# Kernel optimization log

Hardware: AMD Instinct MI355X
Metric: run time of the kernel (lower is better)

## Reference

```python
import jax, jax.numpy as jnp
import numpy as np

B, S, IN, N, OUT = 16, 4096, 256, 256, 256
EPS = 1e-5

def setup_inputs() -> dict:
    key = jax.random.key(0)
    ks = jax.random.split(key, 6)
    return {
        "u": jax.random.normal(ks[0], (B, S, IN), dtype=jnp.float32),
        "A": jax.random.normal(ks[1], (N, N), dtype=jnp.float32) * 0.05,
        "B_w": jax.random.normal(ks[2], (N, IN), dtype=jnp.float32) * (1.0 / np.sqrt(IN)),
        "B_b": jax.random.normal(ks[3], (N,), dtype=jnp.float32) * 0.01,
        "ln_g": jnp.ones((N,), dtype=jnp.float32),
        "ln_b": jnp.zeros((N,), dtype=jnp.float32),
        "C_w": jax.random.normal(ks[4], (OUT, N), dtype=jnp.float32) * (1.0 / np.sqrt(N)),
        "C_b": jax.random.normal(ks[5], (OUT,), dtype=jnp.float32) * 0.01,
    }

def _layernorm(x, g, b):
    mu = jnp.mean(x, axis=-1, keepdims=True)
    var = jnp.mean(jnp.square(x - mu), axis=-1, keepdims=True)
    return (x - mu) * jax.lax.rsqrt(var + EPS) * g + b

def reference(u, A, B_w, B_b, ln_g, ln_b, C_w, C_b):
    # Precompute input injection B(u_t) for all t: [B, S, N]
    Bu = jnp.einsum('bsi,ni->bsn', u, B_w) + B_b
    state0 = jnp.zeros((u.shape[0], A.shape[0]), dtype=u.dtype)

    def step(state, bu_t):
        s = state @ A.T + bu_t          # [B, N]
        s = _layernorm(s, ln_g, ln_b)
        s = jax.nn.relu(s)
        return s, s

    _, states_t = jax.lax.scan(step, state0, jnp.swapaxes(Bu, 0, 1))  # [S, B, N]
    states = jnp.swapaxes(states_t, 0, 1)                              # [B, S, N]
    outputs = jnp.einsum('bsn,on->bso', states, C_w) + C_b             # [B, S, OUT]
    return states, outputs
```

## Files before the change

kernel.cpp:

```cpp
#include <hip/hip_runtime.h>

#define B_DIM 16
#define S_DIM 4096
#define N_DIM 256
#define EPS 1e-5f

__global__ __launch_bounds__(256)
void gemm_xwT_bias(const float* __restrict__ X,
                   const float* __restrict__ W,
                   const float* __restrict__ bias,
                   float* __restrict__ Y,
                   int M)
{
    __shared__ float Xs[16][68];
    __shared__ float Ws[16][68];

    const int tid = threadIdx.x;
    const int m0 = blockIdx.x * 64;
    const int n0 = blockIdx.y * 64;
    const int tx = tid & 15;
    const int ty = tid >> 4;

    float acc[4][4] = {};

    for (int k0 = 0; k0 < 256; k0 += 16) {
        {
            const int r  = tid >> 2;
            const int kk = (tid & 3) * 4;
            float4 v = *(const float4*)(X + (size_t)(m0 + r) * 256 + k0 + kk);
            Xs[kk + 0][r] = v.x; Xs[kk + 1][r] = v.y;
            Xs[kk + 2][r] = v.z; Xs[kk + 3][r] = v.w;
            float4 w = *(const float4*)(W + (size_t)(n0 + r) * 256 + k0 + kk);
            Ws[kk + 0][r] = w.x; Ws[kk + 1][r] = w.y;
            Ws[kk + 2][r] = w.z; Ws[kk + 3][r] = w.w;
        }
        __syncthreads();

        #pragma unroll
        for (int k = 0; k < 16; ++k) {
            float4 xv = *(const float4*)&Xs[k][ty * 4];
            float4 wv = *(const float4*)&Ws[k][tx * 4];
            float xa[4] = {xv.x, xv.y, xv.z, xv.w};
            float wa[4] = {wv.x, wv.y, wv.z, wv.w};
            #pragma unroll
            for (int i = 0; i < 4; ++i)
                #pragma unroll
                for (int j = 0; j < 4; ++j)
                    acc[i][j] += xa[i] * wa[j];
        }
        __syncthreads();
    }

    const int nbase = n0 + tx * 4;
    float4 bv = *(const float4*)(bias + nbase);
    #pragma unroll
    for (int i = 0; i < 4; ++i) {
        const int m = m0 + ty * 4 + i;
        float4 o;
        o.x = acc[i][0] + bv.x;
        o.y = acc[i][1] + bv.y;
        o.z = acc[i][2] + bv.z;
        o.w = acc[i][3] + bv.w;
        *(float4*)(Y + (size_t)m * 256 + nbase) = o;
    }
}

template<int CTRL>
__device__ __forceinline__ float dpp_term(float x) {
    return __int_as_float(
        __builtin_amdgcn_update_dpp(0, __float_as_int(x), CTRL, 0xF, 0xF, true));
}

__device__ __forceinline__ float wave_sum_l63(float v) {
    v += dpp_term<0x111>(v);
    v += dpp_term<0x112>(v);
    v += dpp_term<0x114>(v);
    v += dpp_term<0x118>(v);
    v += dpp_term<0x142>(v);
    v += dpp_term<0x143>(v);
    return v;
}

__device__ __forceinline__ float readlane63(float x) {
    return __int_as_float(__builtin_amdgcn_readlane(__float_as_int(x), 63));
}

__global__ __launch_bounds__(512, 2)
void scan_kernel(const float* __restrict__ A,
                 const float* __restrict__ Bu,
                 const float* __restrict__ ln_g,
                 const float* __restrict__ ln_b,
                 float* __restrict__ states)
{
    const int b = blockIdx.x;
    const int t = threadIdx.x;
    const int w = t >> 6;
    const int l = t & 63;

    __shared__ float s_state[256];
    __shared__ float s_partial[8][256];

    float4 a4[4][8];
    #pragma unroll
    for (int j = 0; j < 4; ++j) {
        const float* arow = A + (size_t)(4 * l + j) * 256 + 32 * w;
        #pragma unroll
        for (int c = 0; c < 8; ++c)
            a4[j][c] = ((const float4*)arow)[c];
    }

    const bool red = (w == 0);

    const float* bu_base  = Bu + (size_t)b * S_DIM * N_DIM;
    float*       out_base = states + (size_t)b * S_DIM * N_DIM;

    float4 g4  = make_float4(0.f, 0.f, 0.f, 0.f);
    float4 be4 = g4;
    float4 bu0 = g4, bu1 = g4;
    if (red) {
        g4  = ((const float4*)ln_g)[l];
        be4 = ((const float4*)ln_b)[l];
        bu0 = ((const float4*)bu_base)[l];
        bu1 = ((const float4*)(bu_base + N_DIM))[l];
        ((float4*)s_state)[l] = make_float4(0.f, 0.f, 0.f, 0.f);
    }
    __syncthreads();

    for (int step = 0; step < S_DIM; ++step) {
        float4 bu2 = make_float4(0.f, 0.f, 0.f, 0.f);
        if (red && (step + 2 < S_DIM))
            bu2 = ((const float4*)(bu_base + (size_t)(step + 2) * N_DIM))[l];

        const float4* sp = (const float4*)(s_state + 32 * w);
        float accA[4] = {0.f, 0.f, 0.f, 0.f};
        float accB[4] = {0.f, 0.f, 0.f, 0.f};
        #pragma unroll
        for (int c = 0; c < 8; ++c) {
            const float4 sc = sp[c];
            #pragma unroll
            for (int j = 0; j < 4; ++j) {
                const float4 a = a4[j][c];
                if (c & 1) {
                    accB[j] = fmaf(a.x, sc.x, accB[j]);
                    accB[j] = fmaf(a.y, sc.y, accB[j]);
                    accB[j] = fmaf(a.z, sc.z, accB[j]);
                    accB[j] = fmaf(a.w, sc.w, accB[j]);
                } else {
                    accA[j] = fmaf(a.x, sc.x, accA[j]);
                    accA[j] = fmaf(a.y, sc.y, accA[j]);
                    accA[j] = fmaf(a.z, sc.z, accA[j]);
                    accA[j] = fmaf(a.w, sc.w, accA[j]);
                }
            }
        }
        float4 pr;
        pr.x = accA[0] + accB[0];
        pr.y = accA[1] + accB[1];
        pr.z = accA[2] + accB[2];
        pr.w = accA[3] + accB[3];
        *(float4*)&s_partial[w][4 * l] = pr;

        asm volatile("s_waitcnt lgkmcnt(0)" ::: "memory");
        __builtin_amdgcn_s_barrier();

        if (red) {
            const float* prow = &s_partial[0][4 * l];
            const float4 q0 = *(const float4*)(prow + 0 * 256);
            const float4 q1 = *(const float4*)(prow + 1 * 256);
            const float4 q2 = *(const float4*)(prow + 2 * 256);
            const float4 q3 = *(const float4*)(prow + 3 * 256);
            const float4 q4 = *(const float4*)(prow + 4 * 256);
            const float4 q5 = *(const float4*)(prow + 5 * 256);
            const float4 q6 = *(const float4*)(prow + 6 * 256);
            const float4 q7 = *(const float4*)(prow + 7 * 256);

            float4 v;
            v.x = ((q0.x + q1.x) + (q2.x + q3.x)) + ((q4.x + q5.x) + (q6.x + q7.x)) + bu0.x;
            v.y = ((q0.y + q1.y) + (q2.y + q3.y)) + ((q4.y + q5.y) + (q6.y + q7.y)) + bu0.y;
            v.z = ((q0.z + q1.z) + (q2.z + q3.z)) + ((q4.z + q5.z) + (q6.z + q7.z)) + bu0.z;
            v.w = ((q0.w + q1.w) + (q2.w + q3.w)) + ((q4.w + q5.w) + (q6.w + q7.w)) + bu0.w;

            const float sv = (v.x + v.y) + (v.z + v.w);
            const float sq = fmaf(v.x, v.x, fmaf(v.y, v.y, fmaf(v.z, v.z, v.w * v.w)));

            const float tot  = readlane63(wave_sum_l63(sv));
            const float tot2 = readlane63(wave_sum_l63(sq));

            const float mu  = tot * (1.0f / 256.0f);
            const float var = tot2 * (1.0f / 256.0f) - mu * mu;
            const float inv = rsqrtf(var + EPS);

            float4 y;
            y.x = fmaxf((v.x - mu) * inv * g4.x + be4.x, 0.0f);
            y.y = fmaxf((v.y - mu) * inv * g4.y + be4.y, 0.0f);
            y.z = fmaxf((v.z - mu) * inv * g4.z + be4.z, 0.0f);
            y.w = fmaxf((v.w - mu) * inv * g4.w + be4.w, 0.0f);

            ((float4*)s_state)[l] = y;
            *(float4*)(out_base + (size_t)step * N_DIM + 4 * l) = y;

            bu0 = bu1;
            bu1 = bu2;
        }

        asm volatile("s_waitcnt lgkmcnt(0)" ::: "memory");
        __builtin_amdgcn_s_barrier();
    }
}

extern "C" void kernel_launch(void* const* d_in, const int* in_sizes, int n_in,
                              void* d_out, int out_size, void* d_ws, size_t ws_size,
                              hipStream_t stream)
{
    const float* u    = (const float*)d_in[0];
    const float* A    = (const float*)d_in[1];
    const float* B_w  = (const float*)d_in[2];
    const float* B_b  = (const float*)d_in[3];
    const float* ln_g = (const float*)d_in[4];
    const float* ln_b = (const float*)d_in[5];
    const float* C_w  = (const float*)d_in[6];
    const float* C_b  = (const float*)d_in[7];

    float* states  = (float*)d_out;
    float* outputs = (float*)d_out + (size_t)B_DIM * S_DIM * N_DIM;

    float* Bu = outputs;

    const int M = B_DIM * S_DIM;

    {
        dim3 grid(M / 64, N_DIM / 64);
        hipLaunchKernelGGL(gemm_xwT_bias, grid, dim3(256), 0, stream,
                           u, B_w, B_b, Bu, M);
    }

    {
        hipLaunchKernelGGL(scan_kernel, dim3(B_DIM), dim3(512), 0, stream,
                           A, Bu, ln_g, ln_b, states);
    }

    {
        dim3 grid(M / 64, N_DIM / 64);
        hipLaunchKernelGGL(gemm_xwT_bias, grid, dim3(256), 0, stream,
                           states, C_w, C_b, outputs, M);
    }
}
```

Before: 3.150 ms.

## Repartition scan matvec across 1024 threads with distributed LayerNorm reduction

Each scan block now runs 1024 threads. Each output row is split across 4 lane groups that reduce with cross-lane shuffles, replacing the layout where 8 waves wrote partial sums to shared memory and a single wave reduced them. LayerNorm statistics are computed per wave with DPP row sums and combined through a small shared array, so every thread normalizes its own element. This removes the serial single-wave reduction phase that ran between barriers. In exchange it uses more threads per block and makes more redundant reads of the statistics array.

```diff
diff --git a/kernel.cpp b/kernel.cpp
--- a/kernel.cpp
+++ b/kernel.cpp
@@ -71,21 +71,15 @@
         __builtin_amdgcn_update_dpp(0, __float_as_int(x), CTRL, 0xF, 0xF, true));
 }
 
-__device__ __forceinline__ float wave_sum_l63(float v) {
+__device__ __forceinline__ float row_sum_l15(float v) {
     v += dpp_term<0x111>(v);
     v += dpp_term<0x112>(v);
     v += dpp_term<0x114>(v);
     v += dpp_term<0x118>(v);
-    v += dpp_term<0x142>(v);
-    v += dpp_term<0x143>(v);
     return v;
 }
 
-__device__ __forceinline__ float readlane63(float x) {
-    return __int_as_float(__builtin_amdgcn_readlane(__float_as_int(x), 63));
-}
-
-__global__ __launch_bounds__(512, 2)
+__global__ __launch_bounds__(1024, 4)
 void scan_kernel(const float* __restrict__ A,
                  const float* __restrict__ Bu,
                  const float* __restrict__ ln_g,
@@ -96,115 +90,99 @@
     const int t = threadIdx.x;
     const int w = t >> 6;
     const int l = t & 63;
-
-    __shared__ float s_state[256];
-    __shared__ float s_partial[8][256];
-
-    float4 a4[4][8];
+    const int r = l >> 4;
+    const int c = l & 15;
+    const int o = 16 * w + c;
+
+    __shared__ __align__(16) float  s4[4 * 68];
+    __shared__ __align__(16) float2 s_red[16];
+
+    float4 a4[16];
+    {
+        const float* arow = A + (size_t)o * 256 + 64 * r;
+        #pragma unroll
+        for (int i = 0; i < 16; ++i)
+            a4[i] = ((const float4*)arow)[i];
+    }
     #pragma unroll
-    for (int j = 0; j < 4; ++j) {
-        const float* arow = A + (size_t)(4 * l + j) * 256 + 32 * w;
-        #pragma unroll
-        for (int c = 0; c < 8; ++c)
-            a4[j][c] = ((const float4*)arow)[c];
-    }
-
-    const bool red = (w == 0);
+    for (int i = 0; i < 16; ++i)
+        asm volatile("" : "+v"(a4[i].x), "+v"(a4[i].y),
+                          "+v"(a4[i].z), "+v"(a4[i].w));
+
+    const float g    = ln_g[o];
+    const float beta = ln_b[o];
 
     const float* bu_base  = Bu + (size_t)b * S_DIM * N_DIM;
     float*       out_base = states + (size_t)b * S_DIM * N_DIM;
 
-    float4 g4  = make_float4(0.f, 0.f, 0.f, 0.f);
-    float4 be4 = g4;
-    float4 bu0 = g4, bu1 = g4;
-    if (red) {
-        g4  = ((const float4*)ln_g)[l];
-        be4 = ((const float4*)ln_b)[l];
-        bu0 = ((const float4*)bu_base)[l];
-        bu1 = ((const float4*)(bu_base + N_DIM))[l];
-        ((float4*)s_state)[l] = make_float4(0.f, 0.f, 0.f, 0.f);
-    }
+    float bu0 = bu_base[o];
+    float bu1 = bu_base[N_DIM + o];
+
+    if (t < 4 * 68) s4[t] = 0.0f;
+
+    const float* sp     = s4 + 68 * r;
+    const int    wr_idx = 68 * (o >> 6) + (o & 63);
+
     __syncthreads();
 
     for (int step = 0; step < S_DIM; ++step) {
-        float4 bu2 = make_float4(0.f, 0.f, 0.f, 0.f);
-        if (red && (step + 2 < S_DIM))
-            bu2 = ((const float4*)(bu_base + (size_t)(step + 2) * N_DIM))[l];
-
-        const float4* sp = (const float4*)(s_state + 32 * w);
-        float accA[4] = {0.f, 0.f, 0.f, 0.f};
-        float accB[4] = {0.f, 0.f, 0.f, 0.f};
-        #pragma unroll
-        for (int c = 0; c < 8; ++c) {
-            const float4 sc = sp[c];
-            #pragma unroll
-            for (int j = 0; j < 4; ++j) {
-                const float4 a = a4[j][c];
-                if (c & 1) {
-                    accB[j] = fmaf(a.x, sc.x, accB[j]);
-                    accB[j] = fmaf(a.y, sc.y, accB[j]);
-                    accB[j] = fmaf(a.z, sc.z, accB[j]);
-                    accB[j] = fmaf(a.w, sc.w, accB[j]);
-                } else {
-                    accA[j] = fmaf(a.x, sc.x, accA[j]);
-                    accA[j] = fmaf(a.y, sc.y, accA[j]);
-                    accA[j] = fmaf(a.z, sc.z, accA[j]);
-                    accA[j] = fmaf(a.w, sc.w, accA[j]);
-                }
+        float bu2 = 0.0f;
+        if (step + 2 < S_DIM)
+            bu2 = bu_base[(size_t)(step + 2) * N_DIM + o];
+
+        float accA = 0.0f, accB = 0.0f;
+        #pragma unroll
+        for (int i = 0; i < 16; ++i) {
+            const float4 sc = *(const float4*)(sp + 4 * i);
+            const float4 a  = a4[i];
+            if (i & 1) {
+                accB = fmaf(a.x, sc.x, accB);
+                accB = fmaf(a.y, sc.y, accB);
+                accB = fmaf(a.z, sc.z, accB);
+                accB = fmaf(a.w, sc.w, accB);
+            } else {
+                accA = fmaf(a.x, sc.x, accA);
+                accA = fmaf(a.y, sc.y, accA);
+                accA = fmaf(a.z, sc.z, accA);
+                accA = fmaf(a.w, sc.w, accA);
             }
         }
-        float4 pr;
-        pr.x = accA[0] + accB[0];
-        pr.y = accA[1] + accB[1];
-        pr.z = accA[2] + accB[2];
-        pr.w = accA[3] + accB[3];
-        *(float4*)&s_partial[w][4 * l] = pr;
+        float acc = accA + accB;
+
+        acc += __shfl_xor(acc, 16, 64);
+        acc += __shfl_xor(acc, 32, 64);
+        const float v = acc + bu0;
+
+        const float sv = row_sum_l15(v);
+        const float sq = row_sum_l15(v * v);
+        if (l == 15)
+            s_red[w] = make_float2(sv, sq);
 
         asm volatile("s_waitcnt lgkmcnt(0)" ::: "memory");
         __builtin_amdgcn_s_barrier();
 
-        if (red) {
-            const float* prow = &s_partial[0][4 * l];
-            const float4 q0 = *(const float4*)(prow + 0 * 256);
-            const float4 q1 = *(const float4*)(prow + 1 * 256);
-            const float4 q2 = *(const float4*)(prow + 2 * 256);
-            const float4 q3 = *(const float4*)(prow + 3 * 256);
-            const float4 q4 = *(const float4*)(prow + 4 * 256);
-            const float4 q5 = *(const float4*)(prow + 5 * 256);
-            const float4 q6 = *(const float4*)(prow + 6 * 256);
-            const float4 q7 = *(const float4*)(prow + 7 * 256);
-
-            float4 v;
-            v.x = ((q0.x + q1.x) + (q2.x + q3.x)) + ((q4.x + q5.x) + (q6.x + q7.x)) + bu0.x;
-            v.y = ((q0.y + q1.y) + (q2.y + q3.y)) + ((q4.y + q5.y) + (q6.y + q7.y)) + bu0.y;
-            v.z = ((q0.z + q1.z) + (q2.z + q3.z)) + ((q4.z + q5.z) + (q6.z + q7.z)) + bu0.z;
-            v.w = ((q0.w + q1.w) + (q2.w + q3.w)) + ((q4.w + q5.w) + (q6.w + q7.w)) + bu0.w;
-
-            const float sv = (v.x + v.y) + (v.z + v.w);
-            const float sq = fmaf(v.x, v.x, fmaf(v.y, v.y, fmaf(v.z, v.z, v.w * v.w)));
-
-            const float tot  = readlane63(wave_sum_l63(sv));
-            const float tot2 = readlane63(wave_sum_l63(sq));
-
-            const float mu  = tot * (1.0f / 256.0f);
-            const float var = tot2 * (1.0f / 256.0f) - mu * mu;
-            const float inv = rsqrtf(var + EPS);
-
-            float4 y;
-            y.x = fmaxf((v.x - mu) * inv * g4.x + be4.x, 0.0f);
-            y.y = fmaxf((v.y - mu) * inv * g4.y + be4.y, 0.0f);
-            y.z = fmaxf((v.z - mu) * inv * g4.z + be4.z, 0.0f);
-            y.w = fmaxf((v.w - mu) * inv * g4.w + be4.w, 0.0f);
-
-            ((float4*)s_state)[l] = y;
-            *(float4*)(out_base + (size_t)step * N_DIM + 4 * l) = y;
-
-            bu0 = bu1;
-            bu1 = bu2;
+        float sumS = 0.0f, sumQ = 0.0f;
+        #pragma unroll
+        for (int j = 0; j < 8; ++j) {
+            const float4 p = ((const float4*)s_red)[j];
+            sumS += p.x + p.z;
+            sumQ += p.y + p.w;
+        }
+        const float mu  = sumS * (1.0f / 256.0f);
+        const float var = sumQ * (1.0f / 256.0f) - mu * mu;
+        const float inv = rsqrtf(var + EPS);
+        const float y   = fmaxf((v - mu) * inv * g + beta, 0.0f);
+
+        if (r == 0) {
+            s4[wr_idx] = y;
+            out_base[(size_t)step * N_DIM + o] = y;
         }
 
         asm volatile("s_waitcnt lgkmcnt(0)" ::: "memory");
         __builtin_amdgcn_s_barrier();
+
+        bu0 = bu1;
+        bu1 = bu2;
     }
 }
 
@@ -235,7 +213,7 @@
     }
 
     {
-        hipLaunchKernelGGL(scan_kernel, dim3(B_DIM), dim3(512), 0, stream,
+        hipLaunchKernelGGL(scan_kernel, dim3(B_DIM), dim3(1024), 0, stream,
                            A, Bu, ln_g, ln_b, states);
     }
 
```

Result: slower. 6.316 ms (+100.5%).
